# Performance work log

Hardware: AMD Instinct MI355X
Metric: run time of the kernel (lower is better)

## Reference

```python
import jax, jax.numpy as jnp
import numpy as np

T, B, I, H = 512, 64, 1024, 1024


def setup_inputs() -> dict:
    key = jax.random.key(0)
    ks = jax.random.split(key, 16)
    d = {
        "inputs": jax.random.normal(ks[0], (T, B, I), dtype=jnp.float32),
        "hx": jnp.zeros((B, H), dtype=jnp.float32),
        "cx": jnp.zeros((B, H), dtype=jnp.float32),
        # weights [H, I] / [H, H] as in nn.Parameter(torch.randn(...)); scaled down for stability
        "w_ii": jax.random.normal(ks[1], (H, I), jnp.float32) * 0.02,
        "w_fi": jax.random.normal(ks[2], (H, I), jnp.float32) * 0.02,
        "w_ai": jax.random.normal(ks[3], (H, I), jnp.float32) * 0.02,
        "w_oi": jax.random.normal(ks[4], (H, I), jnp.float32) * 0.02,
        "w_ih": jax.random.normal(ks[5], (H, H), jnp.float32) * 0.02,
        "w_fh": jax.random.normal(ks[6], (H, H), jnp.float32) * 0.02,
        "w_ah": jax.random.normal(ks[7], (H, H), jnp.float32) * 0.02,
        "w_oh": jax.random.normal(ks[8], (H, H), jnp.float32) * 0.02,
        "b_i": jax.random.uniform(ks[9], (H,), jnp.float32),
        "b_f": jax.random.uniform(ks[10], (H,), jnp.float32),
        "b_a": jax.random.uniform(ks[11], (H,), jnp.float32),
        "b_o": jax.random.normal(ks[12], (H,), jnp.float32),
    }
    return d


def reference(inputs, hx, cx, w_ii, w_fi, w_ai, w_oi, w_ih, w_fh, w_ah, w_oh,
              b_i, b_f, b_a, b_o):
    # FP quant type -> weight proxies and quant activations are identity;
    # layer_norm='identity'; rec_quant/out_quant are IdentityQuant.
    # Stack the 4 gate matrices so each step does one [B,I]x[I,4H] and one
    # [B,H]x[H,4H] GEMM (same math as the 8 separate torch.mm calls).
    Wi = jnp.concatenate([w_ii, w_fi, w_ai, w_oi], axis=0).T  # [I, 4H]
    Wh = jnp.concatenate([w_ih, w_fh, w_ah, w_oh], axis=0).T  # [H, 4H]
    b = jnp.concatenate([b_i, b_f, b_a, b_o], axis=0)          # [4H]
    Hh = hx.shape[-1]

    def step(carry, x_t):
        h, c = carry
        gates = x_t @ Wi + h @ Wh + b                 # [B, 4H]
        i_g, f_g, a_g, o_g = jnp.split(gates, 4, axis=-1)
        i_g = jax.nn.sigmoid(i_g)
        f_g = jax.nn.sigmoid(f_g)
        a_g = jnp.tanh(a_g)
        o_g = jax.nn.sigmoid(o_g)
        cy = f_g * c + i_g * a_g
        hy = o_g * jnp.tanh(cy)
        return (hy, cy), hy

    (hy, cy), outputs = jax.lax.scan(step, (hx, cx), inputs)
    return outputs, hy, cy
```

## Files before the change

kernel.cpp:

```cpp
#include <hip/hip_runtime.h>
#include <cstdint>

typedef _Float16 half8 __attribute__((ext_vector_type(8)));
typedef _Float16 half4v __attribute__((ext_vector_type(4)));
typedef float floatx4 __attribute__((ext_vector_type(4)));
typedef unsigned long long u64;

__device__ __forceinline__ float sig_(float x) { return 1.f / (1.f + __expf(-x)); }
__device__ __forceinline__ float tanh_(float x) {
  x = fminf(15.f, fmaxf(-15.f, x));
  float e = __expf(2.f * x);
  return (e - 1.f) / (e + 1.f);
}

__global__ void cvt_x_kernel(const float* __restrict__ x, _Float16* __restrict__ xh, int n) {
  int i = (blockIdx.x * 256 + threadIdx.x) * 4;
  if (i < n) {
    const float4 v = *(const float4*)(x + i);
    half4v o = {(_Float16)v.x, (_Float16)v.y, (_Float16)v.z, (_Float16)v.w};
    *(half4v*)(xh + i) = o;
  }
}

__global__ void build_w_kernel(const float* w0, const float* w1, const float* w2, const float* w3,
                               const float* w4, const float* w5, const float* w6, const float* w7,
                               const float* b0, const float* b1, const float* b2, const float* b3,
                               _Float16* __restrict__ Wip, _Float16* __restrict__ Whp,
                               float* __restrict__ biasp) {
  int n = blockIdx.x;
  if (n < 8192) {
    const float* srcs[8] = {w0, w1, w2, w3, w4, w5, w6, w7};
    int which = n >> 12;
    int row = n & 4095;
    int u = row >> 2, g = row & 3;
    const float* s = srcs[which * 4 + g] + (size_t)u * 1024;
    _Float16* dst = (which ? Whp : Wip) + (size_t)row * 1024;
    int t = threadIdx.x * 4;
    float4 v = *(const float4*)(s + t);
    half4v o = {(_Float16)v.x, (_Float16)v.y, (_Float16)v.z, (_Float16)v.w};
    *(half4v*)(dst + t) = o;
  } else {
    const float* bs[4] = {b0, b1, b2, b3};
    for (int idx = threadIdx.x; idx < 4096; idx += 256)
      biasp[idx] = bs[idx & 3][idx >> 2];
  }
}

__global__ void init_h_kernel(const float* __restrict__ hx, unsigned int* __restrict__ hbuf) {
  int i = blockIdx.x * 256 + threadIdx.x;
  if (i < 32768) {
    unsigned short lo = __builtin_bit_cast(unsigned short, (_Float16)hx[2 * i]);
    unsigned short hi = __builtin_bit_cast(unsigned short, (_Float16)hx[2 * i + 1]);
    hbuf[i] = (unsigned int)lo | ((unsigned int)hi << 16);
  }
}

__global__ void zero_flags_kernel(unsigned int* __restrict__ flags) {
  int i = blockIdx.x * 256 + threadIdx.x;
  if (i < 8192) flags[i] = 0u;
}

__global__ __launch_bounds__(256) void gemm_g_kernel(const _Float16* __restrict__ Xh,
                                                     const _Float16* __restrict__ Wp,
                                                     const float* __restrict__ biasp,
                                                     _Float16* __restrict__ G3) {
  __shared__ _Float16 Al[4][128][8];
  __shared__ _Float16 Bl[4][128][8];
  const int tid = threadIdx.x;
  const int w = tid >> 6, l = tid & 63;
  const int wm = (w >> 1) * 64, wn = (w & 1) * 64;
  const int ml = l & 15, kg = l >> 4;
  const int bm = blockIdx.x, bn = blockIdx.y;
  const int r0 = tid & 127, kc0 = tid >> 7;
  const int kc1 = kc0 + 2;
  const size_t arow0 = (size_t)(bm * 128 + r0) * 1024;
  const size_t brow0 = (size_t)(bn * 128 + r0) * 1024;
  floatx4 acc[4][4] = {};
  for (int kt = 0; kt < 1024; kt += 32) {
    __syncthreads();
    __builtin_amdgcn_global_load_lds(
        (const __attribute__((address_space(1))) unsigned int*)(Xh + arow0 + kt + kc0 * 8),
        (__attribute__((address_space(3))) unsigned int*)&Al[kc0][r0][0], 16, 0, 0);
    __builtin_amdgcn_global_load_lds(
        (const __attribute__((address_space(1))) unsigned int*)(Xh + arow0 + kt + kc1 * 8),
        (__attribute__((address_space(3))) unsigned int*)&Al[kc1][r0][0], 16, 0, 0);
    __builtin_amdgcn_global_load_lds(
        (const __attribute__((address_space(1))) unsigned int*)(Wp + brow0 + kt + kc0 * 8),
        (__attribute__((address_space(3))) unsigned int*)&Bl[kc0][r0][0], 16, 0, 0);
    __builtin_amdgcn_global_load_lds(
        (const __attribute__((address_space(1))) unsigned int*)(Wp + brow0 + kt + kc1 * 8),
        (__attribute__((address_space(3))) unsigned int*)&Bl[kc1][r0][0], 16, 0, 0);
    __syncthreads();
    half8 af[4], bf[4];
#pragma unroll
    for (int i = 0; i < 4; ++i) af[i] = *(const half8*)&Al[kg][wm + i * 16 + ml][0];
#pragma unroll
    for (int j = 0; j < 4; ++j) bf[j] = *(const half8*)&Bl[kg][wn + j * 16 + ml][0];
#pragma unroll
    for (int i = 0; i < 4; ++i)
#pragma unroll
      for (int j = 0; j < 4; ++j)
        acc[i][j] = __builtin_amdgcn_mfma_f32_16x16x32_f16(af[i], bf[j], acc[i][j], 0, 0, 0);
  }
  const int t = (bm * 128 + wm) >> 6;
#pragma unroll
  for (int j = 0; j < 4; ++j) {
    const int col = bn * 128 + wn + j * 16 + ml;
    const float bj = biasp[col];
    const int p = col >> 4;
#pragma unroll
    for (int i = 0; i < 4; ++i) {
      half4v pk = {(_Float16)(acc[i][j][0] + bj), (_Float16)(acc[i][j][1] + bj),
                   (_Float16)(acc[i][j][2] + bj), (_Float16)(acc[i][j][3] + bj)};
      *(half4v*)&G3[((size_t)p * 512 + t) * 1024 + i * 256 + kg * 64 + ml * 4] = pk;
    }
  }
}

__global__ __launch_bounds__(256, 1) void lstm_rec_kernel(
    const _Float16* __restrict__ G3, const _Float16* __restrict__ Whp,
    unsigned int* __restrict__ hbuf, const float* __restrict__ cx,
    float* __restrict__ out, unsigned int* __restrict__ flags) {
  const int P = blockIdx.x, tid = threadIdx.x;
  const int kw = tid >> 6, l = tid & 63;
  const int ml = l & 15, kg = l >> 4;
  const int bg = P >> 6, ug = P & 63;
  __shared__ float pacc[4][16][68];

  half8 wfr[32];
#pragma unroll
  for (int cgt = 0; cgt < 4; ++cgt)
#pragma unroll
    for (int s = 0; s < 8; ++s)
      wfr[cgt * 8 + s] =
          *(const half8*)&Whp[(size_t)(64 * ug + 16 * cgt + ml) * 1024 + (8 * kw + s) * 32 + kg * 8];

  const int b16 = tid >> 4, u16 = tid & 15;
  const int batch = 16 * bg + b16, U = 16 * ug + u16;
  float c = cx[batch * 1024 + U];
  const size_t gbase = ((size_t)(4 * ug + kw) * 512) * 1024 + bg * 256 + kg * 64 + ml * 4;
  u64 ginb = *(const u64*)&G3[gbase];
  __syncthreads();

  for (int t = 0; t < 512; ++t) {
    const u64* hq = (const u64*)(hbuf + (size_t)(t & 1) * 32768);
    u64* hnq = (u64*)(hbuf + (size_t)((t & 1) ^ 1) * 32768);

    u64 cp[16];
#pragma unroll
    for (int s = 0; s < 8; ++s) {
      const size_t base = (size_t)(16 * bg + ml) * 256 + 64 * kw + 8 * s + 2 * kg;
      cp[2 * s] = __hip_atomic_load(&hq[base], __ATOMIC_RELAXED, __HIP_MEMORY_SCOPE_AGENT);
      cp[2 * s + 1] =
          __hip_atomic_load(&hq[base + 1], __ATOMIC_RELAXED, __HIP_MEMORY_SCOPE_AGENT);
    }

    floatx4 acc[4] = {};
#pragma unroll
    for (int s = 0; s < 8; ++s) {
      union { u64 q[2]; half8 h; } au;
      au.q[0] = cp[2 * s];
      au.q[1] = cp[2 * s + 1];
#pragma unroll
      for (int cgt = 0; cgt < 4; ++cgt)
        acc[cgt] = __builtin_amdgcn_mfma_f32_16x16x32_f16(au.h, wfr[cgt * 8 + s], acc[cgt], 0, 0, 0);
    }

    union { u64 q; half4v h4; } gu; gu.q = ginb;
#pragma unroll
    for (int cgt = 0; cgt < 4; ++cgt) {
#pragma unroll
      for (int r = 0; r < 4; ++r) {
        float v = acc[cgt][r];
        if (cgt == kw) v += (float)gu.h4[r];
        pacc[kw][kg * 4 + r][16 * cgt + ml] = v;
      }
    }
    __syncthreads();

    floatx4 ssum = *(const floatx4*)&pacc[0][b16][4 * u16];
#pragma unroll
    for (int kw2 = 1; kw2 < 4; ++kw2)
      ssum += *(const floatx4*)&pacc[kw2][b16][4 * u16];

    const float ig = sig_(ssum[0]), fg = sig_(ssum[1]);
    const float ag = tanh_(ssum[2]), og = sig_(ssum[3]);
    c = fg * c + ig * ag;
    const float h = og * tanh_(c);

    unsigned int mine = (unsigned int)__builtin_bit_cast(unsigned short, (_Float16)h);
    unsigned int pair = mine | (((unsigned int)__shfl_xor((int)mine, 1)) << 16);
    u64 quad = (u64)pair | ((u64)(unsigned int)__shfl_xor((int)pair, 2) << 32);
    if ((u16 & 3) == 0)
      __hip_atomic_store(&hnq[(size_t)batch * 256 + 4 * ug + (u16 >> 2)], quad,
                         __ATOMIC_RELAXED, __HIP_MEMORY_SCOPE_AGENT);

    if (t == 511) {
      out[(size_t)t * 65536 + batch * 1024 + U] = h;
      out[(size_t)33554432 + batch * 1024 + U] = h;
      out[(size_t)33619968 + batch * 1024 + U] = c;
      break;
    }

    __builtin_amdgcn_s_waitcnt(0x0F70);
    __syncthreads();
    if (tid == 0)
      __hip_atomic_store(&flags[P * 32], (unsigned)(t + 1), __ATOMIC_RELAXED,
                         __HIP_MEMORY_SCOPE_AGENT);
    out[(size_t)t * 65536 + batch * 1024 + U] = h;
    const u64 gnext = *(const u64*)&G3[gbase + (size_t)(t + 1) * 1024];
    const unsigned tgt = (unsigned)(t + 1);
    int done;
    do {
      unsigned v = tgt;
      if (tid < 64)
        v = __hip_atomic_load(&flags[(bg * 64 + tid) * 32], __ATOMIC_RELAXED,
                              __HIP_MEMORY_SCOPE_AGENT);
      done = __syncthreads_and((int)(v >= tgt));
      if (!done) __builtin_amdgcn_s_sleep(2);
    } while (!done);
    asm volatile("" ::: "memory");
    ginb = gnext;
  }
}

extern "C" void kernel_launch(void* const* d_in, const int* in_sizes, int n_in,
                              void* d_out, int out_size, void* d_ws, size_t ws_size,
                              hipStream_t stream) {
  const float* x    = (const float*)d_in[0];
  const float* hx   = (const float*)d_in[1];
  const float* cxp  = (const float*)d_in[2];
  const float* w_ii = (const float*)d_in[3];
  const float* w_fi = (const float*)d_in[4];
  const float* w_ai = (const float*)d_in[5];
  const float* w_oi = (const float*)d_in[6];
  const float* w_ih = (const float*)d_in[7];
  const float* w_fh = (const float*)d_in[8];
  const float* w_ah = (const float*)d_in[9];
  const float* w_oh = (const float*)d_in[10];
  const float* b_i  = (const float*)d_in[11];
  const float* b_f  = (const float*)d_in[12];
  const float* b_a  = (const float*)d_in[13];
  const float* b_o  = (const float*)d_in[14];
  float* out = (float*)d_out;

  char* ws = (char*)d_ws;
  _Float16* Xh        = (_Float16*)(ws);
  unsigned int* flags = (unsigned int*)(ws);
  _Float16* Wip       = (_Float16*)(ws + 67108864);
  _Float16* Whp       = (_Float16*)(ws + 75497472);
  float* biasp        = (float*)(ws + 83886080);
  unsigned int* hbuf  = (unsigned int*)(ws + 83902464);
  _Float16* G3        = (_Float16*)(ws + 84164864);
  if (ws_size < (size_t)84164864 + 268435456) return;

  cvt_x_kernel<<<32768, 256, 0, stream>>>(x, Xh, 33554432);
  build_w_kernel<<<8193, 256, 0, stream>>>(w_ii, w_fi, w_ai, w_oi, w_ih, w_fh, w_ah, w_oh,
                                           b_i, b_f, b_a, b_o, Wip, Whp, biasp);
  init_h_kernel<<<128, 256, 0, stream>>>(hx, hbuf);
  gemm_g_kernel<<<dim3(256, 32), 256, 0, stream>>>(Xh, Wip, biasp, G3);
  zero_flags_kernel<<<32, 256, 0, stream>>>(flags);
  lstm_rec_kernel<<<256, 256, 0, stream>>>(G3, Whp, hbuf, cxp, out, flags);
}
```

Measured before the change: 3.158 ms.

## Replace per-step flag barrier with sentinel-filled per-timestep hidden-state buffers

Drops the flag-based cross-block barrier. Each timestep's hidden state now goes to its own slot in a large buffer that is prefilled with a NaN sentinel, and consumers spin on their own loaded h values until none equal the sentinel. This removes the flag store, the flag polling, the full-block syncthreads_and loop and the waitcnt fence from each step of the serial recurrence. In exchange it adds a 64MB sentinel fill pass, and correctness now depends on a computed h never equalling the sentinel pattern and on relaxed 64-bit stores becoming visible atomically.

```diff
diff --git a/kernel.cpp b/kernel.cpp
--- a/kernel.cpp
+++ b/kernel.cpp
@@ -46,18 +46,19 @@
   }
 }
 
-__global__ void init_h_kernel(const float* __restrict__ hx, unsigned int* __restrict__ hbuf) {
+__global__ void init_h_kernel(const float* __restrict__ hx, unsigned int* __restrict__ h0) {
   int i = blockIdx.x * 256 + threadIdx.x;
   if (i < 32768) {
     unsigned short lo = __builtin_bit_cast(unsigned short, (_Float16)hx[2 * i]);
     unsigned short hi = __builtin_bit_cast(unsigned short, (_Float16)hx[2 * i + 1]);
-    hbuf[i] = (unsigned int)lo | ((unsigned int)hi << 16);
-  }
-}
-
-__global__ void zero_flags_kernel(unsigned int* __restrict__ flags) {
-  int i = blockIdx.x * 256 + threadIdx.x;
-  if (i < 8192) flags[i] = 0u;
+    h0[i] = (unsigned int)lo | ((unsigned int)hi << 16);
+  }
+}
+
+__global__ void sent_fill_kernel(u64* __restrict__ Hq) {
+  size_t i = ((size_t)blockIdx.x * 256 + threadIdx.x) * 4 + 16384;
+  const u64 s = 0x7FFF7FFF7FFF7FFFull;
+  if (i < 8388608) { Hq[i] = s; Hq[i + 1] = s; Hq[i + 2] = s; Hq[i + 3] = s; }
 }
 
 __global__ __launch_bounds__(256) void gemm_g_kernel(const _Float16* __restrict__ Xh,
@@ -119,12 +120,13 @@
 
 __global__ __launch_bounds__(256, 1) void lstm_rec_kernel(
     const _Float16* __restrict__ G3, const _Float16* __restrict__ Whp,
-    unsigned int* __restrict__ hbuf, const float* __restrict__ cx,
-    float* __restrict__ out, unsigned int* __restrict__ flags) {
+    u64* __restrict__ Hq, const float* __restrict__ cx,
+    float* __restrict__ out) {
   const int P = blockIdx.x, tid = threadIdx.x;
   const int kw = tid >> 6, l = tid & 63;
   const int ml = l & 15, kg = l >> 4;
   const int bg = P >> 6, ug = P & 63;
+  const unsigned SENT32 = 0x7FFF7FFFu;
   __shared__ float pacc[4][16][68];
 
   half8 wfr[32];
@@ -140,19 +142,29 @@
   float c = cx[batch * 1024 + U];
   const size_t gbase = ((size_t)(4 * ug + kw) * 512) * 1024 + bg * 256 + kg * 64 + ml * 4;
   u64 ginb = *(const u64*)&G3[gbase];
+  const size_t lbase = (size_t)(16 * bg + ml) * 256 + 64 * kw + 2 * kg;
   __syncthreads();
 
   for (int t = 0; t < 512; ++t) {
-    const u64* hq = (const u64*)(hbuf + (size_t)(t & 1) * 32768);
-    u64* hnq = (u64*)(hbuf + (size_t)((t & 1) ^ 1) * 32768);
+    const u64* hs = Hq + (size_t)t * 16384;
 
     u64 cp[16];
 #pragma unroll
-    for (int s = 0; s < 8; ++s) {
-      const size_t base = (size_t)(16 * bg + ml) * 256 + 64 * kw + 8 * s + 2 * kg;
-      cp[2 * s] = __hip_atomic_load(&hq[base], __ATOMIC_RELAXED, __HIP_MEMORY_SCOPE_AGENT);
-      cp[2 * s + 1] =
-          __hip_atomic_load(&hq[base + 1], __ATOMIC_RELAXED, __HIP_MEMORY_SCOPE_AGENT);
+    for (int i = 0; i < 16; ++i)
+      cp[i] = __hip_atomic_load(&hs[lbase + 8 * (i >> 1) + (i & 1)], __ATOMIC_RELAXED,
+                                __HIP_MEMORY_SCOPE_AGENT);
+    for (;;) {
+      int myok = 1;
+#pragma unroll
+      for (int i = 0; i < 16; ++i)
+        myok &= ((unsigned)cp[i] != SENT32) & ((unsigned)(cp[i] >> 32) != SENT32);
+      if (__all(myok)) break;
+      __builtin_amdgcn_s_sleep(1);
+#pragma unroll
+      for (int i = 0; i < 16; ++i)
+        if (((unsigned)cp[i] == SENT32) | ((unsigned)(cp[i] >> 32) == SENT32))
+          cp[i] = __hip_atomic_load(&hs[lbase + 8 * (i >> 1) + (i & 1)], __ATOMIC_RELAXED,
+                                    __HIP_MEMORY_SCOPE_AGENT);
     }
 
     floatx4 acc[4] = {};
@@ -182,6 +194,7 @@
 #pragma unroll
     for (int kw2 = 1; kw2 < 4; ++kw2)
       ssum += *(const floatx4*)&pacc[kw2][b16][4 * u16];
+    __syncthreads();
 
     const float ig = sig_(ssum[0]), fg = sig_(ssum[1]);
     const float ag = tanh_(ssum[2]), og = sig_(ssum[3]);
@@ -191,9 +204,6 @@
     unsigned int mine = (unsigned int)__builtin_bit_cast(unsigned short, (_Float16)h);
     unsigned int pair = mine | (((unsigned int)__shfl_xor((int)mine, 1)) << 16);
     u64 quad = (u64)pair | ((u64)(unsigned int)__shfl_xor((int)pair, 2) << 32);
-    if ((u16 & 3) == 0)
-      __hip_atomic_store(&hnq[(size_t)batch * 256 + 4 * ug + (u16 >> 2)], quad,
-                         __ATOMIC_RELAXED, __HIP_MEMORY_SCOPE_AGENT);
 
     if (t == 511) {
       out[(size_t)t * 65536 + batch * 1024 + U] = h;
@@ -202,25 +212,13 @@
       break;
     }
 
-    __builtin_amdgcn_s_waitcnt(0x0F70);
-    __syncthreads();
-    if (tid == 0)
-      __hip_atomic_store(&flags[P * 32], (unsigned)(t + 1), __ATOMIC_RELAXED,
-                         __HIP_MEMORY_SCOPE_AGENT);
+    if ((u16 & 3) == 0)
+      __hip_atomic_store(&Hq[(size_t)(t + 1) * 16384 + (size_t)batch * 256 + 4 * ug + (u16 >> 2)],
+                         quad, __ATOMIC_RELAXED, __HIP_MEMORY_SCOPE_AGENT);
+
     out[(size_t)t * 65536 + batch * 1024 + U] = h;
-    const u64 gnext = *(const u64*)&G3[gbase + (size_t)(t + 1) * 1024];
-    const unsigned tgt = (unsigned)(t + 1);
-    int done;
-    do {
-      unsigned v = tgt;
-      if (tid < 64)
-        v = __hip_atomic_load(&flags[(bg * 64 + tid) * 32], __ATOMIC_RELAXED,
-                              __HIP_MEMORY_SCOPE_AGENT);
-      done = __syncthreads_and((int)(v >= tgt));
-      if (!done) __builtin_amdgcn_s_sleep(2);
-    } while (!done);
+    ginb = *(const u64*)&G3[gbase + (size_t)(t + 1) * 1024];
     asm volatile("" ::: "memory");
-    ginb = gnext;
   }
 }
 
@@ -246,19 +244,18 @@
 
   char* ws = (char*)d_ws;
   _Float16* Xh        = (_Float16*)(ws);
-  unsigned int* flags = (unsigned int*)(ws);
+  u64* Hq             = (u64*)(ws);
   _Float16* Wip       = (_Float16*)(ws + 67108864);
   _Float16* Whp       = (_Float16*)(ws + 75497472);
   float* biasp        = (float*)(ws + 83886080);
-  unsigned int* hbuf  = (unsigned int*)(ws + 83902464);
   _Float16* G3        = (_Float16*)(ws + 84164864);
   if (ws_size < (size_t)84164864 + 268435456) return;
 
   cvt_x_kernel<<<32768, 256, 0, stream>>>(x, Xh, 33554432);
   build_w_kernel<<<8193, 256, 0, stream>>>(w_ii, w_fi, w_ai, w_oi, w_ih, w_fh, w_ah, w_oh,
                                            b_i, b_f, b_a, b_o, Wip, Whp, biasp);
-  init_h_kernel<<<128, 256, 0, stream>>>(hx, hbuf);
   gemm_g_kernel<<<dim3(256, 32), 256, 0, stream>>>(Xh, Wip, biasp, G3);
-  zero_flags_kernel<<<32, 256, 0, stream>>>(flags);
-  lstm_rec_kernel<<<256, 256, 0, stream>>>(G3, Whp, hbuf, cxp, out, flags);
-}
+  sent_fill_kernel<<<8176, 256, 0, stream>>>(Hq);
+  init_h_kernel<<<128, 256, 0, stream>>>(hx, (unsigned int*)Hq);
+  lstm_rec_kernel<<<256, 256, 0, stream>>>(G3, Whp, Hq, cxp, out);
+}
```

After: 3.093 ms. 2.1% less time.
